# Optimization experiments

Hardware: AMD Instinct MI355X
Metric: run time of the kernel (lower is better)

Reference implementation:

```python
import jax, jax.numpy as jnp
import numpy as np

WS = (4, 4, 4)          # window size (D, H, W)
DIM = 96
HEADS = 8
HEAD_DIM = DIM // HEADS
SCALE = HEAD_DIM ** (-0.5)
N = WS[0] * WS[1] * WS[2]  # 64 tokens per window


def _relative_position_index(ws):
    coords = np.stack(np.meshgrid(np.arange(ws[0]), np.arange(ws[1]), np.arange(ws[2]), indexing='ij'))
    cf = coords.reshape(3, -1)                       # [3, N]
    rel = cf[:, :, None] - cf[:, None, :]            # [3, N, N]
    rel = rel.transpose(1, 2, 0).astype(np.int64)    # [N, N, 3]
    rel[:, :, 0] += ws[0] - 1
    rel[:, :, 1] += ws[1] - 1
    rel[:, :, 2] += ws[2] - 1
    rel[:, :, 0] *= (2 * ws[1] - 1) * (2 * ws[2] - 1)
    rel[:, :, 1] *= 2 * ws[2] - 1
    return jnp.asarray(rel.sum(-1))                  # [N, N]

REL_IDX = _relative_position_index(WS)


def setup_inputs() -> dict:
    key = jax.random.key(0)
    ks = jax.random.split(key, 6)
    B = 4096   # total windows (64 images x 64 windows)
    nW = 64
    table_size = (2 * WS[0] - 1) * (2 * WS[1] - 1) * (2 * WS[2] - 1)  # 343
    return {
        'x': jax.random.normal(ks[0], (B, N, DIM), jnp.float32),
        'mask': jax.random.normal(ks[1], (nW, N, N), jnp.float32),
        'qkv_w': jax.random.normal(ks[2], (3 * DIM, DIM), jnp.float32) * 0.02,
        'proj_w': jax.random.normal(ks[3], (DIM, DIM), jnp.float32) * 0.02,
        'proj_b': jnp.zeros((DIM,), jnp.float32),
        'bias_table': jax.random.normal(ks[4], (table_size, HEADS), jnp.float32) * 0.02,
    }


def reference(x, mask, qkv_w, proj_w, proj_b, bias_table):
    B, n, C = x.shape
    # QKV projection (torch Linear: y = x @ W.T), split into heads
    qkv = (x @ qkv_w.T).reshape(B, n, 3, HEADS, HEAD_DIM)
    qkv = jnp.transpose(qkv, (2, 0, 3, 1, 4))        # [3, B, H, N, hd]
    q, k, v = qkv[0], qkv[1], qkv[2]
    attn = jnp.einsum('bhnd,bhmd->bhnm', q, k) * SCALE
    # gathered relative position bias: [N, N, H] -> [H, N, N]
    bias = bias_table[REL_IDX[:n, :n].reshape(-1)].reshape(n, n, HEADS)
    attn = attn + jnp.transpose(bias, (2, 0, 1))[None]
    # shifted-window mask add
    nW = mask.shape[0]
    attn = attn.reshape(B // nW, nW, HEADS, n, n) + mask[None, :, None]
    attn = attn.reshape(B, HEADS, n, n)
    attn = jax.nn.softmax(attn, axis=-1)
    out = jnp.einsum('bhnm,bhmd->bnhd', attn, v).reshape(B, n, C)
    return out @ proj_w.T + proj_b
```

## Files before the change

### kernel.cpp

```cpp
#include <hip/hip_runtime.h>
#include <stdint.h>


typedef float  f32x4  __attribute__((ext_vector_type(4)));
typedef float  f32x16 __attribute__((ext_vector_type(16)));
typedef short  short8 __attribute__((ext_vector_type(8)));

#define WS_WQKV_OFF  (8388608)
#define WS_WPROJ_OFF (8388608 + 55296)

__device__ __forceinline__ unsigned short f2bf(float f) {
  union { float f; uint32_t u; } v; v.f = f;
  uint32_t u = v.u + 0x7fffu + ((v.u >> 16) & 1u);
  return (unsigned short)(u >> 16);
}

__global__ void prep_weights(const float* __restrict__ qkv_w,
                             const float* __restrict__ proj_w,
                             unsigned short* __restrict__ ws16) {
  int tid = blockIdx.x * 256 + threadIdx.x;
  if (tid < 27648) {
    float v = qkv_w[tid];
    if (tid < 9216) v *= 0.28867513459481288f;
    ws16[WS_WQKV_OFF / 2 + tid] = f2bf(v);
  } else {
    int t = tid - 27648;
    ws16[WS_WPROJ_OFF / 2 + t] = f2bf(proj_w[t]);
  }
}

__global__ void prep_biasm(const float* __restrict__ mask,
                           const float* __restrict__ bias_table,
                           float* __restrict__ biasm) {
  int tid = blockIdx.x * 256 + threadIdx.x;
  int m = tid & 63;
  int r = (tid >> 6) & 63;
  int h = (tid >> 12) & 7;
  int w = tid >> 15;
  int dr = r >> 4, hr = (r >> 2) & 3, wr = r & 3;
  int dm = m >> 4, hm = (m >> 2) & 3, wm = m & 3;
  int idx = (dr - dm + 3) * 49 + (hr - hm + 3) * 7 + (wr - wm + 3);
  biasm[tid] = bias_table[idx * 8 + h] + mask[(w * 64 + r) * 64 + m];
}

__global__ __launch_bounds__(256, 2) void attn_main(
    const float* __restrict__ x, const float* __restrict__ proj_b,
    const unsigned short* __restrict__ ws16, const float* __restrict__ biasm,
    float* __restrict__ out) {
  __shared__ __align__(16) unsigned short xo[64][104];
  __shared__ __align__(16) unsigned short q_s[8][64][24];
  __shared__ __align__(16) unsigned short k_s[8][64][24];
  __shared__ __align__(16) unsigned short v_s[8][16][72];

  const int tid  = threadIdx.x;
  const int wv   = tid >> 6;
  const int lane = tid & 63;
  const int lo4 = lane & 15, hi4 = lane >> 4;
  const int lo5 = lane & 31, hi5 = lane >> 5;
  const int blk = blockIdx.x;
  const int wmask = blk & 63;

  const unsigned short* wqkv  = ws16 + WS_WQKV_OFF / 2;
  const unsigned short* wproj = ws16 + WS_WPROJ_OFF / 2;

  for (int i = tid; i < 512; i += 256) {
    int h = i >> 6, r = i & 63;
    *(uint2*)&q_s[h][r][12] = make_uint2(0u, 0u);
    *(uint2*)&k_s[h][r][12] = make_uint2(0u, 0u);
  }

  {
    const float4* xsrc = (const float4*)(x + (size_t)blk * (64 * 96));
    for (int i = tid; i < 1536; i += 256) {
      float4 v = xsrc[i];
      int t = i / 24, c4 = (i % 24) * 4;
      uint2 pk;
      pk.x = (uint32_t)f2bf(v.x) | ((uint32_t)f2bf(v.y) << 16);
      pk.y = (uint32_t)f2bf(v.z) | ((uint32_t)f2bf(v.w) << 16);
      *(uint2*)&xo[t][c4] = pk;
    }
  }
  __syncthreads();

  {
    f32x4 acc[18];
#pragma unroll
    for (int nt = 0; nt < 18; ++nt) acc[nt] = (f32x4){0.f, 0.f, 0.f, 0.f};
    const int arow = wv * 16 + lo4;
#pragma unroll
    for (int ks = 0; ks < 3; ++ks) {
      short8 af = *(const short8*)&xo[arow][ks * 32 + hi4 * 8];
#pragma unroll
      for (int nt = 0; nt < 18; ++nt) {
        short8 bf = *(const short8*)&wqkv[(nt * 16 + lo4) * 96 + ks * 32 + hi4 * 8];
        acc[nt] = __builtin_amdgcn_mfma_f32_16x16x32_bf16(af, bf, acc[nt], 0, 0, 0);
      }
    }
#pragma unroll
    for (int nt = 0; nt < 18; ++nt) {
      const int o = nt * 16 + lo4;
      const int rem = o - (nt >= 12 ? 192 : (nt >= 6 ? 96 : 0));
      const int head = rem / 12;
      const int ch = rem - head * 12;
#pragma unroll
      for (int j = 0; j < 4; ++j) {
        const int r = wv * 16 + hi4 * 4 + j;
        unsigned short bv = f2bf(acc[nt][j]);
        if (nt < 6)       q_s[head][r][ch] = bv;
        else if (nt < 12) k_s[head][r][ch] = bv;
        else              v_s[head][ch][r] = bv;
      }
    }
  }
  __syncthreads();

  for (int it = 0; it < 2; ++it) {
    const int h = wv * 2 + it;
    const float* bm = biasm + (size_t)(wmask * 8 + h) * 4096;

    f32x16 c[2][2];
#pragma unroll
    for (int ti = 0; ti < 2; ++ti)
#pragma unroll
      for (int tj = 0; tj < 2; ++tj)
#pragma unroll
        for (int q4 = 0; q4 < 4; ++q4) {
          float4 b4 = *(const float4*)&bm[(tj * 32 + lo5) * 64 + ti * 32 + 8 * q4 + 4 * hi5];
          c[ti][tj][4 * q4 + 0] = b4.x;
          c[ti][tj][4 * q4 + 1] = b4.y;
          c[ti][tj][4 * q4 + 2] = b4.z;
          c[ti][tj][4 * q4 + 3] = b4.w;
        }
#pragma unroll
    for (int ti = 0; ti < 2; ++ti) {
      short8 af = *(const short8*)&k_s[h][ti * 32 + lo5][hi5 * 8];
#pragma unroll
      for (int tj = 0; tj < 2; ++tj) {
        short8 bf = *(const short8*)&q_s[h][tj * 32 + lo5][hi5 * 8];
        c[ti][tj] = __builtin_amdgcn_mfma_f32_32x32x16_bf16(af, bf, c[ti][tj], 0, 0, 0);
      }
    }

#pragma unroll
    for (int tj = 0; tj < 2; ++tj) {
      float mx = -1e30f;
#pragma unroll
      for (int ti = 0; ti < 2; ++ti)
#pragma unroll
        for (int reg = 0; reg < 16; ++reg) mx = fmaxf(mx, c[ti][tj][reg]);
      mx = fmaxf(mx, __shfl_xor(mx, 32));
      float sum = 0.f;
#pragma unroll
      for (int ti = 0; ti < 2; ++ti)
#pragma unroll
        for (int reg = 0; reg < 16; ++reg) {
          float e = __expf(c[ti][tj][reg] - mx);
          c[ti][tj][reg] = e;
          sum += e;
        }
      sum += __shfl_xor(sum, 32);
      float rs = 1.0f / sum;
#pragma unroll
      for (int ti = 0; ti < 2; ++ti)
#pragma unroll
        for (int reg = 0; reg < 16; ++reg) c[ti][tj][reg] *= rs;
    }

    uint32_t pk[2][2][8];
#pragma unroll
    for (int ti = 0; ti < 2; ++ti)
#pragma unroll
      for (int tj = 0; tj < 2; ++tj)
#pragma unroll
        for (int u = 0; u < 8; ++u)
          pk[ti][tj][u] = (uint32_t)f2bf(c[ti][tj][2 * u]) |
                          ((uint32_t)f2bf(c[ti][tj][2 * u + 1]) << 16);

    f32x16 oD[2];
    oD[0] = (f32x16)(0.f); oD[1] = (f32x16)(0.f);
#pragma unroll
    for (int kc = 0; kc < 4; ++kc) {
      const int ti = kc >> 1, base = 4 * (kc & 1);
      short8 av = *(const short8*)&v_s[h][lo5 & 15][kc * 16 + hi5 * 8];
#pragma unroll
      for (int tj = 0; tj < 2; ++tj) {
        uint32_t A0 = pk[ti][tj][base + 0], A1 = pk[ti][tj][base + 1];
        uint32_t A2 = pk[ti][tj][base + 2], A3 = pk[ti][tj][base + 3];
        uint32_t k0 = hi5 ? A2 : A0, k1 = hi5 ? A3 : A1;
        uint32_t s0 = (uint32_t)__shfl_xor((int)(hi5 ? A0 : A2), 32);
        uint32_t s1 = (uint32_t)__shfl_xor((int)(hi5 ? A1 : A3), 32);
        union { uint32_t u[4]; short8 s; } bfr;
        bfr.u[0] = hi5 ? s0 : k0;
        bfr.u[1] = hi5 ? s1 : k1;
        bfr.u[2] = hi5 ? k0 : s0;
        bfr.u[3] = hi5 ? k1 : s1;
        oD[tj] = __builtin_amdgcn_mfma_f32_32x32x16_bf16(av, bfr.s, oD[tj], 0, 0, 0);
      }
    }

#pragma unroll
    for (int tj = 0; tj < 2; ++tj) {
      const int q = tj * 32 + lo5;
#pragma unroll
      for (int reg = 0; reg < 8; ++reg) {
        const int q4 = reg >> 2, r2 = reg & 3;
        if (q4 == 0) {
          xo[q][h * 12 + r2 + 4 * hi5] = f2bf(oD[tj][reg]);
        } else if (hi5 == 0) {
          xo[q][h * 12 + 8 + r2] = f2bf(oD[tj][reg]);
        }
      }
    }
  }
  __syncthreads();

  {
    f32x4 acc[6];
#pragma unroll
    for (int nt = 0; nt < 6; ++nt) acc[nt] = (f32x4){0.f, 0.f, 0.f, 0.f};
    const int arow = wv * 16 + lo4;
#pragma unroll
    for (int ks = 0; ks < 3; ++ks) {
      short8 af = *(const short8*)&xo[arow][ks * 32 + hi4 * 8];
#pragma unroll
      for (int nt = 0; nt < 6; ++nt) {
        short8 bf = *(const short8*)&wproj[(nt * 16 + lo4) * 96 + ks * 32 + hi4 * 8];
        acc[nt] = __builtin_amdgcn_mfma_f32_16x16x32_bf16(af, bf, acc[nt], 0, 0, 0);
      }
    }
    float* od = out + (size_t)blk * (64 * 96);
#pragma unroll
    for (int nt = 0; nt < 6; ++nt) {
      float pb = proj_b[nt * 16 + lo4];
#pragma unroll
      for (int j = 0; j < 4; ++j)
        od[(wv * 16 + hi4 * 4 + j) * 96 + nt * 16 + lo4] = acc[nt][j] + pb;
    }
  }
}

extern "C" void kernel_launch(void* const* d_in, const int* in_sizes, int n_in,
                              void* d_out, int out_size, void* d_ws, size_t ws_size,
                              hipStream_t stream) {
  const float* x          = (const float*)d_in[0];
  const float* mask       = (const float*)d_in[1];
  const float* qkv_w      = (const float*)d_in[2];
  const float* proj_w     = (const float*)d_in[3];
  const float* proj_b     = (const float*)d_in[4];
  const float* bias_table = (const float*)d_in[5];

  float* biasm = (float*)d_ws;
  unsigned short* ws16 = (unsigned short*)d_ws;

  prep_weights<<<144, 256, 0, stream>>>(qkv_w, proj_w, ws16);
  prep_biasm<<<8192, 256, 0, stream>>>(mask, bias_table, biasm);
  attn_main<<<4096, 256, 0, stream>>>(x, proj_b, ws16, biasm, (float*)d_out);
}
```

Baseline: 177.9 us.

## Use 512-thread blocks with one wave per head and split GEMM work

Doubles the block to 8 waves so each wave handles one attention head instead of looping over two. The QKV and output projection GEMMs are split across waves by row tile and column group. The aim is more in-flight waves per window to hide latency and shorten each block's critical path. The cost is tighter per-thread register limits under launch_bounds(512,4), which may cause spills.

```diff
diff --git a/kernel.cpp b/kernel.cpp
--- a/kernel.cpp
+++ b/kernel.cpp
@@ -43,7 +43,7 @@
   biasm[tid] = bias_table[idx * 8 + h] + mask[(w * 64 + r) * 64 + m];
 }
 
-__global__ __launch_bounds__(256, 2) void attn_main(
+__global__ __launch_bounds__(512, 4) void attn_main(
     const float* __restrict__ x, const float* __restrict__ proj_b,
     const unsigned short* __restrict__ ws16, const float* __restrict__ biasm,
     float* __restrict__ out) {
@@ -63,15 +63,15 @@
   const unsigned short* wqkv  = ws16 + WS_WQKV_OFF / 2;
   const unsigned short* wproj = ws16 + WS_WPROJ_OFF / 2;
 
-  for (int i = tid; i < 512; i += 256) {
-    int h = i >> 6, r = i & 63;
+  {
+    int h = tid >> 6, r = tid & 63;
     *(uint2*)&q_s[h][r][12] = make_uint2(0u, 0u);
     *(uint2*)&k_s[h][r][12] = make_uint2(0u, 0u);
   }
 
   {
     const float4* xsrc = (const float4*)(x + (size_t)blk * (64 * 96));
-    for (int i = tid; i < 1536; i += 256) {
+    for (int i = tid; i < 1536; i += 512) {
       float4 v = xsrc[i];
       int t = i / 24, c4 = (i % 24) * 4;
       uint2 pk;
@@ -83,39 +83,42 @@
   __syncthreads();
 
   {
-    f32x4 acc[18];
-#pragma unroll
-    for (int nt = 0; nt < 18; ++nt) acc[nt] = (f32x4){0.f, 0.f, 0.f, 0.f};
-    const int arow = wv * 16 + lo4;
+    const int mt = wv & 3;
+    const int ng = wv >> 2;
+    f32x4 acc[9];
+#pragma unroll
+    for (int nt = 0; nt < 9; ++nt) acc[nt] = (f32x4){0.f, 0.f, 0.f, 0.f};
+    const int arow = mt * 16 + lo4;
 #pragma unroll
     for (int ks = 0; ks < 3; ++ks) {
       short8 af = *(const short8*)&xo[arow][ks * 32 + hi4 * 8];
 #pragma unroll
-      for (int nt = 0; nt < 18; ++nt) {
-        short8 bf = *(const short8*)&wqkv[(nt * 16 + lo4) * 96 + ks * 32 + hi4 * 8];
+      for (int nt = 0; nt < 9; ++nt) {
+        const int ntg = ng * 9 + nt;
+        short8 bf = *(const short8*)&wqkv[(ntg * 16 + lo4) * 96 + ks * 32 + hi4 * 8];
         acc[nt] = __builtin_amdgcn_mfma_f32_16x16x32_bf16(af, bf, acc[nt], 0, 0, 0);
       }
     }
 #pragma unroll
-    for (int nt = 0; nt < 18; ++nt) {
-      const int o = nt * 16 + lo4;
-      const int rem = o - (nt >= 12 ? 192 : (nt >= 6 ? 96 : 0));
+    for (int nt = 0; nt < 9; ++nt) {
+      const int o = (ng * 9 + nt) * 16 + lo4;
+      const int rem = o - (o >= 192 ? 192 : (o >= 96 ? 96 : 0));
       const int head = rem / 12;
       const int ch = rem - head * 12;
 #pragma unroll
       for (int j = 0; j < 4; ++j) {
-        const int r = wv * 16 + hi4 * 4 + j;
+        const int r = mt * 16 + hi4 * 4 + j;
         unsigned short bv = f2bf(acc[nt][j]);
-        if (nt < 6)       q_s[head][r][ch] = bv;
-        else if (nt < 12) k_s[head][r][ch] = bv;
-        else              v_s[head][ch][r] = bv;
+        if (o < 96)        q_s[head][r][ch] = bv;
+        else if (o < 192)  k_s[head][r][ch] = bv;
+        else               v_s[head][ch][r] = bv;
       }
     }
   }
   __syncthreads();
 
-  for (int it = 0; it < 2; ++it) {
-    const int h = wv * 2 + it;
+  {
+    const int h = wv;
     const float* bm = biasm + (size_t)(wmask * 8 + h) * 4096;
 
     f32x16 c[2][2];
@@ -215,26 +218,30 @@
   __syncthreads();
 
   {
-    f32x4 acc[6];
-#pragma unroll
-    for (int nt = 0; nt < 6; ++nt) acc[nt] = (f32x4){0.f, 0.f, 0.f, 0.f};
-    const int arow = wv * 16 + lo4;
+    const int mt = wv >> 1;
+    const int nb = (wv & 1) * 3;
+    f32x4 acc[3];
+#pragma unroll
+    for (int nt = 0; nt < 3; ++nt) acc[nt] = (f32x4){0.f, 0.f, 0.f, 0.f};
+    const int arow = mt * 16 + lo4;
 #pragma unroll
     for (int ks = 0; ks < 3; ++ks) {
       short8 af = *(const short8*)&xo[arow][ks * 32 + hi4 * 8];
 #pragma unroll
-      for (int nt = 0; nt < 6; ++nt) {
-        short8 bf = *(const short8*)&wproj[(nt * 16 + lo4) * 96 + ks * 32 + hi4 * 8];
+      for (int nt = 0; nt < 3; ++nt) {
+        const int ntg = nb + nt;
+        short8 bf = *(const short8*)&wproj[(ntg * 16 + lo4) * 96 + ks * 32 + hi4 * 8];
         acc[nt] = __builtin_amdgcn_mfma_f32_16x16x32_bf16(af, bf, acc[nt], 0, 0, 0);
       }
     }
     float* od = out + (size_t)blk * (64 * 96);
 #pragma unroll
-    for (int nt = 0; nt < 6; ++nt) {
-      float pb = proj_b[nt * 16 + lo4];
+    for (int nt = 0; nt < 3; ++nt) {
+      const int ntg = nb + nt;
+      float pb = proj_b[ntg * 16 + lo4];
 #pragma unroll
       for (int j = 0; j < 4; ++j)
-        od[(wv * 16 + hi4 * 4 + j) * 96 + nt * 16 + lo4] = acc[nt][j] + pb;
+        od[(mt * 16 + hi4 * 4 + j) * 96 + ntg * 16 + lo4] = acc[nt][j] + pb;
     }
   }
 }
@@ -254,5 +261,5 @@
 
   prep_weights<<<144, 256, 0, stream>>>(qkv_w, proj_w, ws16);
   prep_biasm<<<8192, 256, 0, stream>>>(mask, bias_table, biasm);
-  attn_main<<<4096, 256, 0, stream>>>(x, proj_b, ws16, biasm, (float*)d_out);
-}
+  attn_main<<<4096, 512, 0, stream>>>(x, proj_b, ws16, biasm, (float*)d_out);
+}
```

Measured after the change: 175.4 us. No clear change (-1.4%).
